# Kernel optimization log

Measured on AMD Instinct MI355X. Metric: run time of the kernel, lower is better.

The kernel has to match this reference:

```python
import jax, jax.numpy as jnp
import numpy as np

N_NODES = 100000
N_EDGES = 800000
D_FEAT = 64
N_HIDDEN = 64
N_CLASSES = 16


def setup_inputs() -> dict:
    key = jax.random.key(0)
    ks = jax.random.split(key, 10)
    s = 1.0 / np.sqrt(N_HIDDEN)
    inp = {
        "x": jax.random.normal(ks[0], (N_NODES, D_FEAT), dtype=jnp.float32),
        "edge_index": jax.random.randint(ks[1], (2, N_EDGES), 0, N_NODES, dtype=jnp.int64)
        if jax.config.jax_enable_x64 else jax.random.randint(ks[1], (2, N_EDGES), 0, N_NODES, dtype=jnp.int32),
        "W1": jax.random.normal(ks[2], (D_FEAT, N_HIDDEN), dtype=jnp.float32) * s,
        "b1": jnp.zeros((N_HIDDEN,), jnp.float32),
        "W2": jax.random.normal(ks[3], (N_HIDDEN, N_HIDDEN), dtype=jnp.float32) * s,
        "b2": jnp.zeros((N_HIDDEN,), jnp.float32),
        "W3": jax.random.normal(ks[4], (N_HIDDEN, N_HIDDEN), dtype=jnp.float32) * s,
        "b3": jnp.zeros((N_HIDDEN,), jnp.float32),
        "Wf1": jax.random.normal(ks[5], (N_HIDDEN, N_HIDDEN), dtype=jnp.float32) * s,
        "bf1": jnp.zeros((N_HIDDEN,), jnp.float32),
        "Wf2": jax.random.normal(ks[6], (N_HIDDEN, N_HIDDEN), dtype=jnp.float32) * s,
        "bf2": jnp.zeros((N_HIDDEN,), jnp.float32),
        "Wf3": jax.random.normal(ks[7], (N_HIDDEN, N_CLASSES), dtype=jnp.float32) * s,
        "bf3": jnp.zeros((N_CLASSES,), jnp.float32),
    }
    return inp


def reference(x, edge_index, W1, b1, W2, b2, W3, b3, Wf1, bf1, Wf2, bf2, Wf3, bf3):
    N = x.shape[0]
    loops = jnp.arange(N, dtype=edge_index.dtype)
    src = jnp.concatenate([edge_index[0], loops])  # [E+N]
    dst = jnp.concatenate([edge_index[1], loops])
    # symmetric GCN normalization with self-loops (edge weight 1)
    deg = jax.ops.segment_sum(jnp.ones(src.shape[0], x.dtype), dst, num_segments=N)
    dis = jax.lax.rsqrt(jnp.maximum(deg, 1.0))  # deg >= 1 due to self-loops
    norm = dis[src] * dis[dst]  # [E+N]

    def gcn(h, W, b):
        h = h @ W  # [N, H]
        msg = h[src] * norm[:, None]  # [E+N, H] gather
        return jax.ops.segment_sum(msg, dst, num_segments=N) + b  # scatter-add

    y = jax.nn.relu(gcn(x, W1, b1))
    y = jax.nn.relu(gcn(y, W2, b2))
    y = jax.nn.relu(gcn(y, W3, b3))
    y = jax.nn.relu(y @ Wf1 + bf1)
    y = jax.nn.relu(y @ Wf2 + bf2)
    y = y @ Wf3 + bf3
    return jax.nn.log_softmax(y, axis=1)
```

## Files before the change

kernel.cpp:

```cpp
#include <hip/hip_runtime.h>
#include <hip/hip_bf16.h>

#define NN 100000
#define NE 800000
#define EBLK 391
#define NBUK 196
#define GH_STRIDE 392

typedef __attribute__((ext_vector_type(8))) short bf16x8;
typedef __attribute__((ext_vector_type(4))) float f32x4;

__device__ __forceinline__ unsigned short f2b(float f) {
  unsigned int x = __float_as_uint(f);
  return (unsigned short)((x + 0x7fffu + ((x >> 16) & 1u)) >> 16);
}
__device__ __forceinline__ float b2f(short us) {
  return __uint_as_float(((unsigned int)(unsigned short)us) << 16);
}
__device__ __forceinline__ void acc8(float* acc, bf16x8 v) {
#pragma unroll
  for (int i = 0; i < 8; ++i) acc[i] += b2f(v[i]);
}

static __global__ __launch_bounds__(256) void k_hist(const int* __restrict__ dst, int* __restrict__ ghistT) {
  __shared__ int hist[NBUK];
  int tid = threadIdx.x, blk = blockIdx.x;
  for (int i = tid; i < NBUK; i += 256) hist[i] = 0;
  __syncthreads();
  int base = blk * 2048;
#pragma unroll
  for (int i = 0; i < 8; ++i) {
    int e = base + tid + 256 * i;
    if (e < NE) atomicAdd(&hist[dst[e] >> 9], 1);
  }
  __syncthreads();
  for (int i = tid; i < NBUK; i += 256) ghistT[i * GH_STRIDE + blk] = hist[i];
}

static __global__ __launch_bounds__(64) void k_gscan(int* __restrict__ ghistT, int* __restrict__ btot) {
  int b = blockIdx.x, lane = threadIdx.x;
  int carry = 0;
#pragma unroll
  for (int c = 0; c < (EBLK + 63) / 64; ++c) {
    int e = c * 64 + lane;
    int v = (e < EBLK) ? ghistT[b * GH_STRIDE + e] : 0;
    int s = v;
    for (int off = 1; off < 64; off <<= 1) {
      int t = __shfl_up(s, off);
      if (lane >= off) s += t;
    }
    if (e < EBLK) ghistT[b * GH_STRIDE + e] = carry + s - v;
    carry += __shfl(s, 63);
  }
  if (lane == 0) btot[b] = carry;
}

static __global__ void k_btot(const int* __restrict__ btot, int* __restrict__ bstart) {
  __shared__ int sd[256];
  int tid = threadIdx.x;
  int v = (tid < NBUK) ? btot[tid] : 0;
  sd[tid] = v;
  __syncthreads();
  for (int off = 1; off < 256; off <<= 1) {
    int t = (tid >= off) ? sd[tid - off] : 0;
    __syncthreads();
    sd[tid] += t;
    __syncthreads();
  }
  if (tid <= NBUK) bstart[tid] = sd[tid] - v;
}

static __global__ __launch_bounds__(256) void k_scatter(const int* __restrict__ src, const int* __restrict__ dst,
                                                        const int* __restrict__ ghistT, const int* __restrict__ bstart,
                                                        int* __restrict__ ebuf) {
  __shared__ int hist[256];
  __shared__ int lstart[256];
  __shared__ int cur[NBUK];
  __shared__ int2 sbuf[2048];
  int tid = threadIdx.x, blk = blockIdx.x;
  hist[tid] = 0;
  __syncthreads();
  int base = blk * 2048;
  int dd[8], ss[8];
#pragma unroll
  for (int i = 0; i < 8; ++i) {
    int e = base + tid + 256 * i;
    if (e < NE) {
      dd[i] = dst[e]; ss[i] = src[e];
      atomicAdd(&hist[dd[i] >> 9], 1);
    } else dd[i] = -1;
  }
  __syncthreads();
  int v = hist[tid];
  lstart[tid] = v;
  __syncthreads();
  for (int off = 1; off < 256; off <<= 1) {
    int t = (tid >= off) ? lstart[tid - off] : 0;
    __syncthreads();
    lstart[tid] += t;
    __syncthreads();
  }
  int excl = lstart[tid] - v;
  __syncthreads();
  lstart[tid] = excl;
  if (tid < NBUK) cur[tid] = 0;
  __syncthreads();
#pragma unroll
  for (int i = 0; i < 8; ++i) {
    if (dd[i] >= 0) {
      int b = dd[i] >> 9;
      int p = atomicAdd(&cur[b], 1);
      sbuf[lstart[b] + p] = make_int2((ss[i] << 9) | (dd[i] & 511), b);
    }
  }
  __syncthreads();
  int m = NE - base; if (m > 2048) m = 2048;
#pragma unroll
  for (int i = 0; i < 8; ++i) {
    int j = tid + 256 * i;
    if (j < m) {
      int2 e = sbuf[j];
      int b = e.y;
      int gpos = bstart[b] + ghistT[b * GH_STRIDE + blk] + (j - lstart[b]);
      ebuf[gpos] = e.x;
    }
  }
}

static __global__ __launch_bounds__(256) void k_bucket(const int* __restrict__ ebuf, const int* __restrict__ bstart,
                                                       int2* __restrict__ rc, float* __restrict__ dis,
                                                       int* __restrict__ col_idx) {
  __shared__ int cnt[512];
  __shared__ int lrs[512];
  __shared__ int sd[256];
  int b = blockIdx.x, tid = threadIdx.x;
  int base_n = b << 9;
  int ebeg = bstart[b], eend = bstart[b + 1];
  int m = eend - ebeg;
  cnt[tid] = 0; cnt[tid + 256] = 0;
  __syncthreads();
  for (int j = tid; j < m; j += 256) atomicAdd(&cnt[ebuf[ebeg + j] & 511], 1);
  __syncthreads();
  int v0 = cnt[2 * tid], v1 = cnt[2 * tid + 1];
  int s = v0 + v1;
  sd[tid] = s;
  __syncthreads();
  for (int off = 1; off < 256; off <<= 1) {
    int t = (tid >= off) ? sd[tid - off] : 0;
    __syncthreads();
    sd[tid] += t;
    __syncthreads();
  }
  int excl = sd[tid] - s;
  lrs[2 * tid] = excl;
  lrs[2 * tid + 1] = excl + v0;
  __syncthreads();
  for (int i = tid; i < 512; i += 256) {
    int n = base_n + i;
    if (n < NN) {
      int c = cnt[i];
      rc[n] = make_int2(ebeg + lrs[i], c);
      dis[n] = 1.0f / sqrtf((float)c + 1.0f);
    }
  }
  for (int i = tid; i < 512; i += 256) cnt[i] = lrs[i];
  __syncthreads();
  for (int j = tid; j < m; j += 256) {
    int e = ebuf[ebeg + j];
    int p = atomicAdd(&cnt[e & 511], 1);
    col_idx[ebeg + p] = e >> 9;
  }
}

static __global__ __launch_bounds__(256) void k_wconv(
    const float* __restrict__ W1, const float* __restrict__ W2, const float* __restrict__ W3,
    const float* __restrict__ Wf1, const float* __restrict__ Wf2, const float* __restrict__ Wf3,
    short* __restrict__ W1t, short* __restrict__ W2t, short* __restrict__ W3t,
    short* __restrict__ Wf1t, short* __restrict__ Wf2t, short* __restrict__ Wf3t) {
  int b = blockIdx.x, tid = threadIdx.x;
  if (b < 5) {
    const float* W = (b == 0) ? W1 : (b == 1) ? W2 : (b == 2) ? W3 : (b == 3) ? Wf1 : Wf2;
    short* Wt = (b == 0) ? W1t : (b == 1) ? W2t : (b == 2) ? W3t : (b == 3) ? Wf1t : Wf2t;
#pragma unroll
    for (int i = 0; i < 16; ++i) {
      int idx = tid + 256 * i;
      int k = idx >> 6, nn = idx & 63;
      Wt[nn * 64 + k] = (short)f2b(W[idx]);
    }
  } else {
#pragma unroll
    for (int i = 0; i < 4; ++i) {
      int idx = tid + 256 * i;
      int k = idx >> 4, nn = idx & 15;
      Wf3t[nn * 64 + k] = (short)f2b(Wf3[idx]);
    }
  }
}

__device__ __forceinline__ bf16x8 load_a_frag_f32(const float* __restrict__ p, bool valid) {
  float4 f0 = valid ? *(const float4*)p : make_float4(0.f, 0.f, 0.f, 0.f);
  float4 f1 = valid ? *(const float4*)(p + 4) : make_float4(0.f, 0.f, 0.f, 0.f);
  bf16x8 a;
  a[0] = (short)f2b(f0.x); a[1] = (short)f2b(f0.y); a[2] = (short)f2b(f0.z); a[3] = (short)f2b(f0.w);
  a[4] = (short)f2b(f1.x); a[5] = (short)f2b(f1.y); a[6] = (short)f2b(f1.z); a[7] = (short)f2b(f1.w);
  return a;
}

__device__ __forceinline__ void mm_body(bf16x8 a0, bf16x8 a1, const short* __restrict__ Wt,
                                        const float* __restrict__ dis, short* __restrict__ out,
                                        int row0, int rlane, int g, int n) {
  f32x4 acc[4];
#pragma unroll
  for (int t = 0; t < 4; ++t) acc[t] = (f32x4){0.f, 0.f, 0.f, 0.f};
#pragma unroll
  for (int t = 0; t < 4; ++t) {
    bf16x8 b0 = *(const bf16x8*)(Wt + (rlane + 16 * t) * 64 + g * 8);
    bf16x8 b1 = *(const bf16x8*)(Wt + (rlane + 16 * t) * 64 + g * 8 + 32);
    acc[t] = __builtin_amdgcn_mfma_f32_16x16x32_bf16(a0, b0, acc[t], 0, 0, 0);
    acc[t] = __builtin_amdgcn_mfma_f32_16x16x32_bf16(a1, b1, acc[t], 0, 0, 0);
  }
#pragma unroll
  for (int r = 0; r < 4; ++r) {
    int gr = row0 + g * 4 + r;
    if (gr < n) {
      float s = dis[gr];
#pragma unroll
      for (int t = 0; t < 4; ++t)
        out[(size_t)gr * 64 + rlane + 16 * t] = (short)f2b(acc[t][r] * s);
    }
  }
}

static __global__ __launch_bounds__(256) void k_mm1(const float* __restrict__ in, const short* __restrict__ Wt,
                                                    const float* __restrict__ dis, short* __restrict__ out, int n) {
  int tid = threadIdx.x;
  int lane = tid & 63, w = tid >> 6;
  int row0 = blockIdx.x * 64 + w * 16;
  int rlane = lane & 15, g = lane >> 4;
  int arow = row0 + rlane;
  bool av = arow < n;
  const float* ap = in + (size_t)arow * 64 + g * 8;
  bf16x8 a0 = load_a_frag_f32(ap, av);
  bf16x8 a1 = load_a_frag_f32(ap + 32, av);
  mm_body(a0, a1, Wt, dis, out, row0, rlane, g, n);
}

__device__ __forceinline__ void agg_to_lds(const short* __restrict__ ht, const int2* __restrict__ rc,
                                           const int* __restrict__ col_idx, const float* __restrict__ dis,
                                           const float* __restrict__ bias, short (*Hsw)[72],
                                           int row0, int lane, int n) {
  int g = lane >> 3, f = lane & 7;
  float4 b0v = *(const float4*)&bias[f * 8];
  float4 b1v = *(const float4*)&bias[f * 8 + 4];
  float bb[8] = {b0v.x, b0v.y, b0v.z, b0v.w, b1v.x, b1v.y, b1v.z, b1v.w};
  int node0 = row0 + g, node1 = row0 + 8 + g;
  bool nv0 = node0 < n, nv1 = node1 < n;
  int2 rc0 = nv0 ? rc[node0] : make_int2(0, 0);
  int2 rc1 = nv1 ? rc[node1] : make_int2(0, 0);
  int beg0 = rc0.x, cnt0 = rc0.y;
  int beg1 = rc1.x, cnt1 = rc1.y;
  float dis0 = nv0 ? dis[node0] : 0.f;
  float dis1 = nv1 ? dis[node1] : 0.f;
  float acc0[8] = {0.f, 0.f, 0.f, 0.f, 0.f, 0.f, 0.f, 0.f};
  float acc1[8] = {0.f, 0.f, 0.f, 0.f, 0.f, 0.f, 0.f, 0.f};
  if (nv0) acc8(acc0, *(const bf16x8*)(ht + (size_t)node0 * 64 + f * 8));
  if (nv1) acc8(acc1, *(const bf16x8*)(ht + (size_t)node1 * 64 + f * 8));
  int cmax = max(cnt0, cnt1);
  for (int base = 0; base < cmax; base += 8) {
    int idx0 = (base + f < cnt0) ? col_idx[beg0 + base + f] : 0;
    int idx1 = (base + f < cnt1) ? col_idx[beg1 + base + f] : 0;
    int m0 = cnt0 - base; m0 = (m0 < 0) ? 0 : ((m0 > 8) ? 8 : m0);
    int m1 = cnt1 - base; m1 = (m1 < 0) ? 0 : ((m1 > 8) ? 8 : m1);
    int mm = (m0 > m1) ? m0 : m1;
    int e = 0;
    for (; e + 1 < mm; e += 2) {
      int s00 = __shfl(idx0, g * 8 + e);
      int s01 = __shfl(idx0, g * 8 + e + 1);
      int s10 = __shfl(idx1, g * 8 + e);
      int s11 = __shfl(idx1, g * 8 + e + 1);
      bf16x8 r00 = *(const bf16x8*)(ht + (size_t)s00 * 64 + f * 8);
      bf16x8 r10 = *(const bf16x8*)(ht + (size_t)s10 * 64 + f * 8);
      bf16x8 r01 = *(const bf16x8*)(ht + (size_t)s01 * 64 + f * 8);
      bf16x8 r11 = *(const bf16x8*)(ht + (size_t)s11 * 64 + f * 8);
      if (e < m0)     acc8(acc0, r00);
      if (e + 1 < m0) acc8(acc0, r01);
      if (e < m1)     acc8(acc1, r10);
      if (e + 1 < m1) acc8(acc1, r11);
    }
    if (e < mm) {
      int s00 = __shfl(idx0, g * 8 + e);
      int s10 = __shfl(idx1, g * 8 + e);
      bf16x8 r00 = *(const bf16x8*)(ht + (size_t)s00 * 64 + f * 8);
      bf16x8 r10 = *(const bf16x8*)(ht + (size_t)s10 * 64 + f * 8);
      if (e < m0) acc8(acc0, r00);
      if (e < m1) acc8(acc1, r10);
    }
  }
  bf16x8 o0, o1;
#pragma unroll
  for (int i = 0; i < 8; ++i) {
    o0[i] = (short)f2b(fmaxf(fmaf(dis0, acc0[i], bb[i]), 0.f));
    o1[i] = (short)f2b(fmaxf(fmaf(dis1, acc1[i], bb[i]), 0.f));
  }
  *(bf16x8*)&Hsw[g][f * 8] = o0;
  *(bf16x8*)&Hsw[8 + g][f * 8] = o1;
}

static __global__ __launch_bounds__(256) void k_aggmm(const short* __restrict__ ht, const int2* __restrict__ rc,
                                                      const int* __restrict__ col_idx, const float* __restrict__ dis,
                                                      const float* __restrict__ bias, const short* __restrict__ Wt,
                                                      short* __restrict__ out, int n) {
  __shared__ __align__(16) short Hs[4][16][72];
  int tid = threadIdx.x;
  int lane = tid & 63, w = tid >> 6;
  int row0 = blockIdx.x * 64 + w * 16;
  agg_to_lds(ht, rc, col_idx, dis, bias, Hs[w], row0, lane, n);
  int rlane = lane & 15, g = lane >> 4;
  bf16x8 a0 = *(const bf16x8*)&Hs[w][rlane][g * 8];
  bf16x8 a1 = *(const bf16x8*)&Hs[w][rlane][g * 8 + 32];
  mm_body(a0, a1, Wt, dis, out, row0, rlane, g, n);
}

static __global__ __launch_bounds__(256) void k_aggdense(const short* __restrict__ ht, const int2* __restrict__ rc,
    const int* __restrict__ col_idx, const float* __restrict__ dis, const float* __restrict__ bias,
    const short* __restrict__ W1t, const float* __restrict__ bf1,
    const short* __restrict__ W2t, const float* __restrict__ bf2,
    const short* __restrict__ W3t, const float* __restrict__ bf3,
    float* __restrict__ out, int n) {
  __shared__ __align__(16) short Hs[4][16][72];
  int tid = threadIdx.x;
  int lane = tid & 63, w = tid >> 6;
  int row0 = blockIdx.x * 64 + w * 16;
  agg_to_lds(ht, rc, col_idx, dis, bias, Hs[w], row0, lane, n);
  int rlane = lane & 15, g = lane >> 4;
  bf16x8 a0 = *(const bf16x8*)&Hs[w][rlane][g * 8];
  bf16x8 a1 = *(const bf16x8*)&Hs[w][rlane][g * 8 + 32];
  f32x4 acc[4];
#pragma unroll
  for (int t = 0; t < 4; ++t) acc[t] = (f32x4){0.f, 0.f, 0.f, 0.f};
#pragma unroll
  for (int t = 0; t < 4; ++t) {
    bf16x8 b0 = *(const bf16x8*)(W1t + (rlane + 16 * t) * 64 + g * 8);
    bf16x8 b1 = *(const bf16x8*)(W1t + (rlane + 16 * t) * 64 + g * 8 + 32);
    acc[t] = __builtin_amdgcn_mfma_f32_16x16x32_bf16(a0, b0, acc[t], 0, 0, 0);
    acc[t] = __builtin_amdgcn_mfma_f32_16x16x32_bf16(a1, b1, acc[t], 0, 0, 0);
  }
#pragma unroll
  for (int t = 0; t < 4; ++t) {
    float bb = bf1[16 * t + rlane];
#pragma unroll
    for (int r = 0; r < 4; ++r)
      Hs[w][g * 4 + r][16 * t + rlane] = (short)f2b(fmaxf(acc[t][r] + bb, 0.f));
  }
  bf16x8 c0 = *(const bf16x8*)&Hs[w][rlane][g * 8];
  bf16x8 c1 = *(const bf16x8*)&Hs[w][rlane][g * 8 + 32];
  f32x4 acc2[4];
#pragma unroll
  for (int t = 0; t < 4; ++t) acc2[t] = (f32x4){0.f, 0.f, 0.f, 0.f};
#pragma unroll
  for (int t = 0; t < 4; ++t) {
    bf16x8 b0 = *(const bf16x8*)(W2t + (rlane + 16 * t) * 64 + g * 8);
    bf16x8 b1 = *(const bf16x8*)(W2t + (rlane + 16 * t) * 64 + g * 8 + 32);
    acc2[t] = __builtin_amdgcn_mfma_f32_16x16x32_bf16(c0, b0, acc2[t], 0, 0, 0);
    acc2[t] = __builtin_amdgcn_mfma_f32_16x16x32_bf16(c1, b1, acc2[t], 0, 0, 0);
  }
#pragma unroll
  for (int t = 0; t < 4; ++t) {
    float bb = bf2[16 * t + rlane];
#pragma unroll
    for (int r = 0; r < 4; ++r)
      Hs[w][g * 4 + r][16 * t + rlane] = (short)f2b(fmaxf(acc2[t][r] + bb, 0.f));
  }
  bf16x8 d0 = *(const bf16x8*)&Hs[w][rlane][g * 8];
  bf16x8 d1 = *(const bf16x8*)&Hs[w][rlane][g * 8 + 32];
  bf16x8 e0 = *(const bf16x8*)(W3t + rlane * 64 + g * 8);
  bf16x8 e1 = *(const bf16x8*)(W3t + rlane * 64 + g * 8 + 32);
  f32x4 z = (f32x4){0.f, 0.f, 0.f, 0.f};
  z = __builtin_amdgcn_mfma_f32_16x16x32_bf16(d0, e0, z, 0, 0, 0);
  z = __builtin_amdgcn_mfma_f32_16x16x32_bf16(d1, e1, z, 0, 0, 0);
  float bsc = bf3[rlane];
#pragma unroll
  for (int r = 0; r < 4; ++r) {
    float zz = z[r] + bsc;
    float mx = zz;
    mx = fmaxf(mx, __shfl_xor(mx, 1));
    mx = fmaxf(mx, __shfl_xor(mx, 2));
    mx = fmaxf(mx, __shfl_xor(mx, 4));
    mx = fmaxf(mx, __shfl_xor(mx, 8));
    float ex = __expf(zz - mx);
    ex += __shfl_xor(ex, 1);
    ex += __shfl_xor(ex, 2);
    ex += __shfl_xor(ex, 4);
    ex += __shfl_xor(ex, 8);
    float lse = mx + __logf(ex);
    int gr = row0 + g * 4 + r;
    if (gr < n) out[(size_t)gr * 16 + rlane] = zz - lse;
  }
}

extern "C" void kernel_launch(void* const* d_in, const int* in_sizes, int n_in,
                              void* d_out, int out_size, void* d_ws, size_t ws_size,
                              hipStream_t stream) {
  (void)in_sizes; (void)n_in; (void)out_size; (void)ws_size;
  const float* x   = (const float*)d_in[0];
  const int*   ei  = (const int*)d_in[1];
  const float* W1  = (const float*)d_in[2];
  const float* b1  = (const float*)d_in[3];
  const float* W2  = (const float*)d_in[4];
  const float* b2  = (const float*)d_in[5];
  const float* W3  = (const float*)d_in[6];
  const float* b3  = (const float*)d_in[7];
  const float* Wf1 = (const float*)d_in[8];
  const float* bf1 = (const float*)d_in[9];
  const float* Wf2 = (const float*)d_in[10];
  const float* bf2 = (const float*)d_in[11];
  const float* Wf3 = (const float*)d_in[12];
  const float* bf3 = (const float*)d_in[13];
  float* outp = (float*)d_out;
  const int* srcp = ei;
  const int* dstp = ei + NE;

  char* ws = (char*)d_ws;
  size_t off = 0;
  auto alloc = [&](size_t bytes) { void* p = ws + off; off = (off + bytes + 255) & ~(size_t)255; return p; };
  int2*  rc     = (int2*)alloc((size_t)NN * 8);
  float* dis    = (float*)alloc((size_t)NN * 4);
  int*   colidx = (int*)alloc((size_t)NE * 4);
  int*   ghistT = (int*)alloc((size_t)NBUK * GH_STRIDE * 4);
  int*   btot   = (int*)alloc(256 * 4);
  int*   bstart = (int*)alloc(256 * 4);
  short* W1t    = (short*)alloc(4096 * 2);
  short* W2t    = (short*)alloc(4096 * 2);
  short* W3t    = (short*)alloc(4096 * 2);
  short* Wf1t   = (short*)alloc(4096 * 2);
  short* Wf2t   = (short*)alloc(4096 * 2);
  short* Wf3t   = (short*)alloc(1024 * 2);
  short* bufA   = (short*)alloc((size_t)NN * 64 * 2);
  short* bufB   = (short*)alloc((size_t)NN * 64 * 2);
  int*   ebuf   = (int*)alloc((size_t)NE * 4);

  int gMM = (NN + 63) / 64;

  k_wconv<<<6, 256, 0, stream>>>(W1, W2, W3, Wf1, Wf2, Wf3, W1t, W2t, W3t, Wf1t, Wf2t, Wf3t);
  k_hist<<<EBLK, 256, 0, stream>>>(dstp, ghistT);
  k_gscan<<<NBUK, 64, 0, stream>>>(ghistT, btot);
  k_btot<<<1, 256, 0, stream>>>(btot, bstart);
  k_scatter<<<EBLK, 256, 0, stream>>>(srcp, dstp, ghistT, bstart, ebuf);
  k_bucket<<<NBUK, 256, 0, stream>>>(ebuf, bstart, rc, dis, colidx);

  k_mm1<<<gMM, 256, 0, stream>>>(x, W1t, dis, bufB, NN);
  k_aggmm<<<gMM, 256, 0, stream>>>(bufB, rc, colidx, dis, b1, W2t, bufA, NN);
  k_aggmm<<<gMM, 256, 0, stream>>>(bufA, rc, colidx, dis, b2, W3t, bufB, NN);
  k_aggdense<<<gMM, 256, 0, stream>>>(bufB, rc, colidx, dis, b3,
                                      Wf1t, bf1, Wf2t, bf2, Wf3t, bf3, outp, NN);
}
```

Before: 152.1 us.

## Replace histogram/scan bucketing with atomic per-bucket slots and shrink aggregation blocks

Removes the k_hist, k_gscan and k_btot kernels. k_scatter now reserves space in each bucket through a global atomic counter, and buckets live in fixed-stride slots of BSTRIDE entries, so the scan passes and their launches go away. Edge order within a bucket is no longer deterministic, and a bucket that holds more than BSTRIDE edges would overflow its slot. The aggregation kernels also move to 128-thread blocks covering 32 rows each, which doubles the grid and is meant to improve load balance.

```diff
diff --git a/kernel.cpp b/kernel.cpp
--- a/kernel.cpp
+++ b/kernel.cpp
@@ -5,7 +5,7 @@
 #define NE 800000
 #define EBLK 391
 #define NBUK 196
-#define GH_STRIDE 392
+#define BSTRIDE 6144
 
 typedef __attribute__((ext_vector_type(8))) short bf16x8;
 typedef __attribute__((ext_vector_type(4))) float f32x4;
@@ -22,59 +22,11 @@
   for (int i = 0; i < 8; ++i) acc[i] += b2f(v[i]);
 }
 
-static __global__ __launch_bounds__(256) void k_hist(const int* __restrict__ dst, int* __restrict__ ghistT) {
-  __shared__ int hist[NBUK];
-  int tid = threadIdx.x, blk = blockIdx.x;
-  for (int i = tid; i < NBUK; i += 256) hist[i] = 0;
-  __syncthreads();
-  int base = blk * 2048;
-#pragma unroll
-  for (int i = 0; i < 8; ++i) {
-    int e = base + tid + 256 * i;
-    if (e < NE) atomicAdd(&hist[dst[e] >> 9], 1);
-  }
-  __syncthreads();
-  for (int i = tid; i < NBUK; i += 256) ghistT[i * GH_STRIDE + blk] = hist[i];
-}
-
-static __global__ __launch_bounds__(64) void k_gscan(int* __restrict__ ghistT, int* __restrict__ btot) {
-  int b = blockIdx.x, lane = threadIdx.x;
-  int carry = 0;
-#pragma unroll
-  for (int c = 0; c < (EBLK + 63) / 64; ++c) {
-    int e = c * 64 + lane;
-    int v = (e < EBLK) ? ghistT[b * GH_STRIDE + e] : 0;
-    int s = v;
-    for (int off = 1; off < 64; off <<= 1) {
-      int t = __shfl_up(s, off);
-      if (lane >= off) s += t;
-    }
-    if (e < EBLK) ghistT[b * GH_STRIDE + e] = carry + s - v;
-    carry += __shfl(s, 63);
-  }
-  if (lane == 0) btot[b] = carry;
-}
-
-static __global__ void k_btot(const int* __restrict__ btot, int* __restrict__ bstart) {
-  __shared__ int sd[256];
-  int tid = threadIdx.x;
-  int v = (tid < NBUK) ? btot[tid] : 0;
-  sd[tid] = v;
-  __syncthreads();
-  for (int off = 1; off < 256; off <<= 1) {
-    int t = (tid >= off) ? sd[tid - off] : 0;
-    __syncthreads();
-    sd[tid] += t;
-    __syncthreads();
-  }
-  if (tid <= NBUK) bstart[tid] = sd[tid] - v;
-}
-
 static __global__ __launch_bounds__(256) void k_scatter(const int* __restrict__ src, const int* __restrict__ dst,
-                                                        const int* __restrict__ ghistT, const int* __restrict__ bstart,
-                                                        int* __restrict__ ebuf) {
+                                                        int* __restrict__ gcur, int* __restrict__ ebuf) {
   __shared__ int hist[256];
   __shared__ int lstart[256];
+  __shared__ int gbase[256];
   __shared__ int cur[NBUK];
   __shared__ int2 sbuf[2048];
   int tid = threadIdx.x, blk = blockIdx.x;
@@ -103,7 +55,10 @@
   int excl = lstart[tid] - v;
   __syncthreads();
   lstart[tid] = excl;
-  if (tid < NBUK) cur[tid] = 0;
+  if (tid < NBUK) {
+    cur[tid] = 0;
+    gbase[tid] = (v > 0) ? atomicAdd(&gcur[tid], v) : 0;
+  }
   __syncthreads();
 #pragma unroll
   for (int i = 0; i < 8; ++i) {
@@ -121,13 +76,13 @@
     if (j < m) {
       int2 e = sbuf[j];
       int b = e.y;
-      int gpos = bstart[b] + ghistT[b * GH_STRIDE + blk] + (j - lstart[b]);
+      int gpos = b * BSTRIDE + gbase[b] + (j - lstart[b]);
       ebuf[gpos] = e.x;
     }
   }
 }
 
-static __global__ __launch_bounds__(256) void k_bucket(const int* __restrict__ ebuf, const int* __restrict__ bstart,
+static __global__ __launch_bounds__(256) void k_bucket(const int* __restrict__ ebuf, const int* __restrict__ gcur,
                                                        int2* __restrict__ rc, float* __restrict__ dis,
                                                        int* __restrict__ col_idx) {
   __shared__ int cnt[512];
@@ -135,8 +90,8 @@
   __shared__ int sd[256];
   int b = blockIdx.x, tid = threadIdx.x;
   int base_n = b << 9;
-  int ebeg = bstart[b], eend = bstart[b + 1];
-  int m = eend - ebeg;
+  int ebeg = b * BSTRIDE;
+  int m = gcur[b];
   cnt[tid] = 0; cnt[tid + 256] = 0;
   __syncthreads();
   for (int j = tid; j < m; j += 256) atomicAdd(&cnt[ebuf[ebeg + j] & 511], 1);
@@ -306,14 +261,14 @@
   *(bf16x8*)&Hsw[8 + g][f * 8] = o1;
 }
 
-static __global__ __launch_bounds__(256) void k_aggmm(const short* __restrict__ ht, const int2* __restrict__ rc,
+static __global__ __launch_bounds__(128) void k_aggmm(const short* __restrict__ ht, const int2* __restrict__ rc,
                                                       const int* __restrict__ col_idx, const float* __restrict__ dis,
                                                       const float* __restrict__ bias, const short* __restrict__ Wt,
                                                       short* __restrict__ out, int n) {
-  __shared__ __align__(16) short Hs[4][16][72];
+  __shared__ __align__(16) short Hs[2][16][72];
   int tid = threadIdx.x;
   int lane = tid & 63, w = tid >> 6;
-  int row0 = blockIdx.x * 64 + w * 16;
+  int row0 = blockIdx.x * 32 + w * 16;
   agg_to_lds(ht, rc, col_idx, dis, bias, Hs[w], row0, lane, n);
   int rlane = lane & 15, g = lane >> 4;
   bf16x8 a0 = *(const bf16x8*)&Hs[w][rlane][g * 8];
@@ -321,16 +276,16 @@
   mm_body(a0, a1, Wt, dis, out, row0, rlane, g, n);
 }
 
-static __global__ __launch_bounds__(256) void k_aggdense(const short* __restrict__ ht, const int2* __restrict__ rc,
+static __global__ __launch_bounds__(128) void k_aggdense(const short* __restrict__ ht, const int2* __restrict__ rc,
     const int* __restrict__ col_idx, const float* __restrict__ dis, const float* __restrict__ bias,
     const short* __restrict__ W1t, const float* __restrict__ bf1,
     const short* __restrict__ W2t, const float* __restrict__ bf2,
     const short* __restrict__ W3t, const float* __restrict__ bf3,
     float* __restrict__ out, int n) {
-  __shared__ __align__(16) short Hs[4][16][72];
+  __shared__ __align__(16) short Hs[2][16][72];
   int tid = threadIdx.x;
   int lane = tid & 63, w = tid >> 6;
-  int row0 = blockIdx.x * 64 + w * 16;
+  int row0 = blockIdx.x * 32 + w * 16;
   agg_to_lds(ht, rc, col_idx, dis, bias, Hs[w], row0, lane, n);
   int rlane = lane & 15, g = lane >> 4;
   bf16x8 a0 = *(const bf16x8*)&Hs[w][rlane][g * 8];
@@ -425,10 +380,8 @@
   auto alloc = [&](size_t bytes) { void* p = ws + off; off = (off + bytes + 255) & ~(size_t)255; return p; };
   int2*  rc     = (int2*)alloc((size_t)NN * 8);
   float* dis    = (float*)alloc((size_t)NN * 4);
-  int*   colidx = (int*)alloc((size_t)NE * 4);
-  int*   ghistT = (int*)alloc((size_t)NBUK * GH_STRIDE * 4);
-  int*   btot   = (int*)alloc(256 * 4);
-  int*   bstart = (int*)alloc(256 * 4);
+  int*   gcur   = (int*)alloc(256 * 4);
+  int*   colidx = (int*)alloc((size_t)NBUK * BSTRIDE * 4);
   short* W1t    = (short*)alloc(4096 * 2);
   short* W2t    = (short*)alloc(4096 * 2);
   short* W3t    = (short*)alloc(4096 * 2);
@@ -437,20 +390,19 @@
   short* Wf3t   = (short*)alloc(1024 * 2);
   short* bufA   = (short*)alloc((size_t)NN * 64 * 2);
   short* bufB   = (short*)alloc((size_t)NN * 64 * 2);
-  int*   ebuf   = (int*)alloc((size_t)NE * 4);
+  int*   ebuf   = (int*)alloc((size_t)NBUK * BSTRIDE * 4);
 
   int gMM = (NN + 63) / 64;
-
+  int gAG = (NN + 31) / 32;
+
+  hipMemsetAsync(gcur, 0, 256 * 4, stream);
   k_wconv<<<6, 256, 0, stream>>>(W1, W2, W3, Wf1, Wf2, Wf3, W1t, W2t, W3t, Wf1t, Wf2t, Wf3t);
-  k_hist<<<EBLK, 256, 0, stream>>>(dstp, ghistT);
-  k_gscan<<<NBUK, 64, 0, stream>>>(ghistT, btot);
-  k_btot<<<1, 256, 0, stream>>>(btot, bstart);
-  k_scatter<<<EBLK, 256, 0, stream>>>(srcp, dstp, ghistT, bstart, ebuf);
-  k_bucket<<<NBUK, 256, 0, stream>>>(ebuf, bstart, rc, dis, colidx);
+  k_scatter<<<EBLK, 256, 0, stream>>>(srcp, dstp, gcur, ebuf);
+  k_bucket<<<NBUK, 256, 0, stream>>>(ebuf, gcur, rc, dis, colidx);
 
   k_mm1<<<gMM, 256, 0, stream>>>(x, W1t, dis, bufB, NN);
-  k_aggmm<<<gMM, 256, 0, stream>>>(bufB, rc, colidx, dis, b1, W2t, bufA, NN);
-  k_aggmm<<<gMM, 256, 0, stream>>>(bufA, rc, colidx, dis, b2, W3t, bufB, NN);
-  k_aggdense<<<gMM, 256, 0, stream>>>(bufB, rc, colidx, dis, b3,
+  k_aggmm<<<gAG, 128, 0, stream>>>(bufB, rc, colidx, dis, b1, W2t, bufA, NN);
+  k_aggmm<<<gAG, 128, 0, stream>>>(bufA, rc, colidx, dis, b2, W3t, bufB, NN);
+  k_aggdense<<<gAG, 128, 0, stream>>>(bufB, rc, colidx, dis, b3,
                                       Wf1t, bf1, Wf2t, bf2, Wf3t, bf3, outp, NN);
 }
```

New measurement: 147.3 us. -3.1%, faster.
